# Performance work log

Measured on AMD Instinct MI355X. Metric: run time of the kernel, lower is better.

The kernel has to match this reference:

```python
import jax, jax.numpy as jnp
import numpy as np

EPS = 1e-8  # torch F.cosine_similarity default eps


def _cos_gram(x):
    # row-normalize with eps-clamped norms, then Gram matrix [N, N]
    norms = jnp.maximum(jnp.linalg.norm(x, axis=1, keepdims=True), EPS)
    xn = x / norms
    return xn @ xn.T


def setup_inputs() -> dict:
    key = jax.random.key(0)
    k1, k2 = jax.random.split(key)
    N, D = 8192, 128
    return {
        "feat_q": jax.random.normal(k1, (N, D), dtype=jnp.float32),
        "feat_k": jax.random.normal(k2, (N, D), dtype=jnp.float32),
    }


def reference(feat_q, feat_k):
    feat_k = jax.lax.stop_gradient(feat_k)  # feat_k.detach()
    N = feat_q.shape[0]
    qsim = _cos_gram(feat_q)  # [N, N]
    ksim = _cos_gram(feat_k)  # [N, N]
    # mean of (qsim - ksim)^2 over all off-diagonal (i != j) pairs
    diff2 = (qsim - ksim) ** 2
    off_diag = ~jnp.eye(N, dtype=bool)
    denom = jnp.asarray(N * (N - 1), dtype=diff2.dtype)
    loss = jnp.sum(jnp.where(off_diag, diff2, 0.0)) / denom
    return loss
```

## Files before the change

kernel.cpp:

```cpp
#include <hip/hip_runtime.h>
#include <hip/hip_bf16.h>

#define NROWS 8192
#define DDIM  128
#define NKCH  64
#define CHN   128
#define NPAIR 10
#define GB_BLOCKS 160
#define NPAD  38

typedef unsigned short ushort_t;
typedef unsigned int   uint_t;
typedef __attribute__((ext_vector_type(8))) short short8;
typedef __attribute__((ext_vector_type(4))) float floatx4;

#define LDS_PTR(p) ((__attribute__((address_space(3))) void*)(p))
#define GLB_PTR(p) ((const __attribute__((address_space(1))) void*)(p))

static __device__ inline ushort_t f2bf(float f) {
    union { float f; uint_t u; } a; a.f = f;
    uint_t u = a.u + 0x7fffu + ((a.u >> 16) & 1u);
    return (ushort_t)(u >> 16);
}

static __device__ inline void pair_decode(int p, int* ti, int* tj) {
    int i = 0, len = 4;
    while (p >= len) { p -= len; len--; i++; }
    *ti = i; *tj = i + p;
}

__global__ __launch_bounds__(256) void norm_t_kernel(
    const float* __restrict__ q, const float* __restrict__ k,
    ushort_t* __restrict__ Gt, double* acc, uint_t* counter)
{
    __shared__ ushort_t lds[256 * NPAD];
    if (blockIdx.x == 0 && threadIdx.x == 0) { *acc = 0.0; *counter = 0u; }

    int b   = blockIdx.x;
    int c   = b >> 2;
    int sub = b & 3;
    int w   = threadIdx.x >> 6;
    int l   = threadIdx.x & 63;
    int h   = l >> 5;
    int li  = l & 31;

    #pragma unroll
    for (int i = 0; i < 4; ++i) {
        int rl  = i * 8 + w * 2 + h;
        int row = b * 32 + rl;
        {
            float4 v = ((const float4*)(q + (size_t)row * DDIM))[li];
            float ss = v.x * v.x + v.y * v.y + v.z * v.z + v.w * v.w;
            #pragma unroll
            for (int o = 16; o > 0; o >>= 1) ss += __shfl_xor(ss, o, 64);
            float inv = rsqrtf(fmaxf(ss, 1e-16f));
            lds[(4 * li + 0) * NPAD + rl] = f2bf(v.x * inv);
            lds[(4 * li + 1) * NPAD + rl] = f2bf(v.y * inv);
            lds[(4 * li + 2) * NPAD + rl] = f2bf(v.z * inv);
            lds[(4 * li + 3) * NPAD + rl] = f2bf(v.w * inv);
        }
        {
            float4 v = ((const float4*)(k + (size_t)row * DDIM))[li];
            float ss = v.x * v.x + v.y * v.y + v.z * v.z + v.w * v.w;
            #pragma unroll
            for (int o = 16; o > 0; o >>= 1) ss += __shfl_xor(ss, o, 64);
            float inv = rsqrtf(fmaxf(ss, 1e-16f));
            lds[(128 + 4 * li + 0) * NPAD + rl] = f2bf(v.x * inv);
            lds[(128 + 4 * li + 1) * NPAD + rl] = f2bf(v.y * inv);
            lds[(128 + 4 * li + 2) * NPAD + rl] = f2bf(v.z * inv);
            lds[(128 + 4 * li + 3) * NPAD + rl] = f2bf(v.w * inv);
        }
    }
    __syncthreads();

    int a = threadIdx.x;
    union { uint_t u32[16]; uint4 v4[4]; } tb;
    #pragma unroll
    for (int t = 0; t < 16; ++t)
        tb.u32[t] = *(const uint_t*)&lds[a * NPAD + 2 * t];

    char* gdst = (char*)Gt + (size_t)(c * 256 + a) * (CHN * 2) + sub * 64;
    #pragma unroll
    for (int g = 0; g < 4; ++g)
        *(uint4*)(gdst + g * 16) = tb.v4[g];
}

__global__ __launch_bounds__(128, 2) void gram_a_kernel(
    const ushort_t* __restrict__ Gt, float* __restrict__ P)
{
    __shared__ ushort_t sA[64 * CHN];
    __shared__ ushort_t sB[64 * CHN];

    int pair = blockIdx.x >> 6;
    int c    = blockIdx.x & 63;
    int ti, tj;
    pair_decode(pair, &ti, &tj);
    int tid = threadIdx.x;

    const char* gA = (const char*)Gt + (size_t)(c * 256 + ti * 64) * (CHN * 2);
    const char* gB = (const char*)Gt + (size_t)(c * 256 + tj * 64) * (CHN * 2);

    #pragma unroll
    for (int it = 0; it < 8; ++it) {
        int ch = it * 128 + tid;
        int row = ch >> 4, phys = ch & 15;
        int logical = phys ^ (row & 7);
        __builtin_amdgcn_global_load_lds(GLB_PTR(gA + row * 256 + logical * 16),
                                         LDS_PTR((char*)sA + ch * 16), 16, 0, 0);
    }
    #pragma unroll
    for (int it = 0; it < 8; ++it) {
        int ch = it * 128 + tid;
        int row = ch >> 4, phys = ch & 15;
        int logical = phys ^ (row & 7);
        __builtin_amdgcn_global_load_lds(GLB_PTR(gB + row * 256 + logical * 16),
                                         LDS_PTR((char*)sB + ch * 16), 16, 0, 0);
    }
    __syncthreads();

    int w    = tid >> 6;
    int l    = tid & 63;
    int m    = l & 15;
    int quad = l >> 4;

    floatx4 accC[2][4];
    #pragma unroll
    for (int at = 0; at < 2; ++at)
        #pragma unroll
        for (int bt = 0; bt < 4; ++bt)
            accC[at][bt] = (floatx4){0.f, 0.f, 0.f, 0.f};

    #pragma unroll
    for (int kp = 0; kp < 4; ++kp) {
        short8 af[2], bf[4];
        #pragma unroll
        for (int at = 0; at < 2; ++at) {
            int ra   = w * 32 + at * 16 + m;
            int phys = (kp * 4 + quad) ^ (ra & 7);
            af[at] = *(const short8*)&sA[ra * CHN + phys * 8];
        }
        #pragma unroll
        for (int bt = 0; bt < 4; ++bt) {
            int rb   = bt * 16 + m;
            int phys = (kp * 4 + quad) ^ (rb & 7);
            bf[bt] = *(const short8*)&sB[rb * CHN + phys * 8];
        }
        #pragma unroll
        for (int at = 0; at < 2; ++at)
            #pragma unroll
            for (int bt = 0; bt < 4; ++bt)
                accC[at][bt] = __builtin_amdgcn_mfma_f32_16x16x32_bf16(af[at], bf[bt], accC[at][bt], 0, 0, 0);
    }

    float* pt = P + ((size_t)pair * NKCH + c) * 4096;
    #pragma unroll
    for (int at = 0; at < 2; ++at)
        #pragma unroll
        for (int bt = 0; bt < 4; ++bt)
            #pragma unroll
            for (int r = 0; r < 4; ++r) {
                int row = w * 32 + at * 16 + quad * 4 + r;
                int col = bt * 16 + m;
                pt[row * 64 + col] = accC[at][bt][r];
            }
}

__global__ __launch_bounds__(256) void gram_b_kernel(
    const float* __restrict__ P, double* acc, uint_t* counter, float* out)
{
    __shared__ float wsum[4];
    int e    = blockIdx.x * 256 + threadIdx.x;
    int pair = e >> 12;
    int idx  = e & 4095;

    float s = 0.f;
    #pragma unroll
    for (int c = 0; c < NKCH; ++c)
        s += P[((size_t)pair * NKCH + c) * 4096 + idx];

    int ti, tj;
    pair_decode(pair, &ti, &tj);
    float wgt = ((ti < 2) == (tj < 2)) ? 1.f : -1.f;
    if (ti != tj) wgt *= 2.f;
    float v = wgt * s * s;

    int w = threadIdx.x >> 6, l = threadIdx.x & 63;
    #pragma unroll
    for (int o = 32; o > 0; o >>= 1) v += __shfl_xor(v, o, 64);
    if (l == 0) wsum[w] = v;
    __syncthreads();
    if (threadIdx.x == 0) {
        double t = (double)wsum[0] + (double)wsum[1] + (double)wsum[2] + (double)wsum[3];
        atomicAdd(acc, t);
        __threadfence();
        uint_t old = atomicAdd(counter, 1u);
        if (old == GB_BLOCKS - 1) {
            double total = atomicAdd(acc, 0.0);
            out[0] = (float)(total * (1.0 / ((double)NROWS * (double)(NROWS - 1))));
        }
    }
}

extern "C" void kernel_launch(void* const* d_in, const int* in_sizes, int n_in,
                              void* d_out, int out_size, void* d_ws, size_t ws_size,
                              hipStream_t stream) {
    const float* q = (const float*)d_in[0];
    const float* k = (const float*)d_in[1];
    float* out = (float*)d_out;

    double*   acc = (double*)d_ws;
    uint_t*   cnt = (uint_t*)((char*)d_ws + 64);
    ushort_t* Gt  = (ushort_t*)((char*)d_ws + 256);
    float*    P   = (float*)((char*)d_ws + 256 + (size_t)NKCH * 256 * CHN * 2);

    norm_t_kernel<<<NROWS / 32, 256, 0, stream>>>(q, k, Gt, acc, cnt);
    gram_a_kernel<<<NPAIR * NKCH, 128, 0, stream>>>(Gt, P);
    gram_b_kernel<<<GB_BLOCKS, 256, 0, stream>>>(P, acc, cnt, out);
}
```

Before: 74.64 us.

## Fuse chunk reduction into gram kernel with atomics and double-buffered chunk loads

Replaces the partial-product buffer and the separate reduction kernel. Each gram block now handles four K-chunks, double-buffering their LDS loads, and accumulates its 64x64 tile into a small shared matrix with float atomics. The last block to finish computes the weighted sum of squares. The norm kernel is retiled to 16 rows per block and zeroes the accumulation matrix. This removes one launch and the large write and re-read of partials, at the cost of heavy atomic contention (16 blocks per element) and a serial final reduction run by a single block.

```diff
diff --git a/kernel.cpp b/kernel.cpp
--- a/kernel.cpp
+++ b/kernel.cpp
@@ -6,8 +6,10 @@
 #define NKCH  64
 #define CHN   128
 #define NPAIR 10
-#define GB_BLOCKS 160
-#define NPAD  38
+#define NGRP  16
+#define CPG   4
+#define K2_BLOCKS (NPAIR * NGRP)
+#define NPAD1 18
 
 typedef unsigned short ushort_t;
 typedef unsigned int   uint_t;
@@ -31,33 +33,34 @@
 
 __global__ __launch_bounds__(256) void norm_t_kernel(
     const float* __restrict__ q, const float* __restrict__ k,
-    ushort_t* __restrict__ Gt, double* acc, uint_t* counter)
+    ushort_t* __restrict__ Gt, float* __restrict__ M, uint_t* counter)
 {
-    __shared__ ushort_t lds[256 * NPAD];
-    if (blockIdx.x == 0 && threadIdx.x == 0) { *acc = 0.0; *counter = 0u; }
+    __shared__ ushort_t lds[256 * NPAD1];
+    if (blockIdx.x < K2_BLOCKS) M[blockIdx.x * 256 + threadIdx.x] = 0.f;
+    if (blockIdx.x == 0 && threadIdx.x == 0) *counter = 0u;
 
     int b   = blockIdx.x;
-    int c   = b >> 2;
-    int sub = b & 3;
+    int c   = b >> 3;
+    int sub = b & 7;
     int w   = threadIdx.x >> 6;
     int l   = threadIdx.x & 63;
     int h   = l >> 5;
     int li  = l & 31;
 
     #pragma unroll
-    for (int i = 0; i < 4; ++i) {
+    for (int i = 0; i < 2; ++i) {
         int rl  = i * 8 + w * 2 + h;
-        int row = b * 32 + rl;
+        int row = b * 16 + rl;
         {
             float4 v = ((const float4*)(q + (size_t)row * DDIM))[li];
             float ss = v.x * v.x + v.y * v.y + v.z * v.z + v.w * v.w;
             #pragma unroll
             for (int o = 16; o > 0; o >>= 1) ss += __shfl_xor(ss, o, 64);
             float inv = rsqrtf(fmaxf(ss, 1e-16f));
-            lds[(4 * li + 0) * NPAD + rl] = f2bf(v.x * inv);
-            lds[(4 * li + 1) * NPAD + rl] = f2bf(v.y * inv);
-            lds[(4 * li + 2) * NPAD + rl] = f2bf(v.z * inv);
-            lds[(4 * li + 3) * NPAD + rl] = f2bf(v.w * inv);
+            lds[(4 * li + 0) * NPAD1 + rl] = f2bf(v.x * inv);
+            lds[(4 * li + 1) * NPAD1 + rl] = f2bf(v.y * inv);
+            lds[(4 * li + 2) * NPAD1 + rl] = f2bf(v.z * inv);
+            lds[(4 * li + 3) * NPAD1 + rl] = f2bf(v.w * inv);
         }
         {
             float4 v = ((const float4*)(k + (size_t)row * DDIM))[li];
@@ -65,58 +68,61 @@
             #pragma unroll
             for (int o = 16; o > 0; o >>= 1) ss += __shfl_xor(ss, o, 64);
             float inv = rsqrtf(fmaxf(ss, 1e-16f));
-            lds[(128 + 4 * li + 0) * NPAD + rl] = f2bf(v.x * inv);
-            lds[(128 + 4 * li + 1) * NPAD + rl] = f2bf(v.y * inv);
-            lds[(128 + 4 * li + 2) * NPAD + rl] = f2bf(v.z * inv);
-            lds[(128 + 4 * li + 3) * NPAD + rl] = f2bf(v.w * inv);
+            lds[(128 + 4 * li + 0) * NPAD1 + rl] = f2bf(v.x * inv);
+            lds[(128 + 4 * li + 1) * NPAD1 + rl] = f2bf(v.y * inv);
+            lds[(128 + 4 * li + 2) * NPAD1 + rl] = f2bf(v.z * inv);
+            lds[(128 + 4 * li + 3) * NPAD1 + rl] = f2bf(v.w * inv);
         }
     }
     __syncthreads();
 
     int a = threadIdx.x;
-    union { uint_t u32[16]; uint4 v4[4]; } tb;
-    #pragma unroll
-    for (int t = 0; t < 16; ++t)
-        tb.u32[t] = *(const uint_t*)&lds[a * NPAD + 2 * t];
-
-    char* gdst = (char*)Gt + (size_t)(c * 256 + a) * (CHN * 2) + sub * 64;
-    #pragma unroll
-    for (int g = 0; g < 4; ++g)
-        *(uint4*)(gdst + g * 16) = tb.v4[g];
-}
-
-__global__ __launch_bounds__(128, 2) void gram_a_kernel(
-    const ushort_t* __restrict__ Gt, float* __restrict__ P)
+    union { uint_t u32[8]; uint4 v4[2]; } tb;
+    #pragma unroll
+    for (int t = 0; t < 8; ++t)
+        tb.u32[t] = *(const uint_t*)&lds[a * NPAD1 + 2 * t];
+
+    char* gdst = (char*)Gt + (size_t)(c * 256 + a) * (CHN * 2) + sub * 32;
+    *(uint4*)(gdst)      = tb.v4[0];
+    *(uint4*)(gdst + 16) = tb.v4[1];
+}
+
+__global__ __launch_bounds__(128) void gram_acc_kernel(
+    const ushort_t* __restrict__ Gt, float* __restrict__ M,
+    uint_t* __restrict__ counter, float* __restrict__ out)
 {
-    __shared__ ushort_t sA[64 * CHN];
-    __shared__ ushort_t sB[64 * CHN];
-
-    int pair = blockIdx.x >> 6;
-    int c    = blockIdx.x & 63;
+    __shared__ ushort_t sA[2][64 * CHN];
+    __shared__ ushort_t sB[2][64 * CHN];
+    __shared__ double dred[2];
+    __shared__ uint_t isLast;
+
+    int pair = blockIdx.x >> 4;
+    int g    = blockIdx.x & 15;
     int ti, tj;
     pair_decode(pair, &ti, &tj);
     int tid = threadIdx.x;
-
-    const char* gA = (const char*)Gt + (size_t)(c * 256 + ti * 64) * (CHN * 2);
-    const char* gB = (const char*)Gt + (size_t)(c * 256 + tj * 64) * (CHN * 2);
-
-    #pragma unroll
-    for (int it = 0; it < 8; ++it) {
-        int ch = it * 128 + tid;
-        int row = ch >> 4, phys = ch & 15;
-        int logical = phys ^ (row & 7);
-        __builtin_amdgcn_global_load_lds(GLB_PTR(gA + row * 256 + logical * 16),
-                                         LDS_PTR((char*)sA + ch * 16), 16, 0, 0);
-    }
-    #pragma unroll
-    for (int it = 0; it < 8; ++it) {
-        int ch = it * 128 + tid;
-        int row = ch >> 4, phys = ch & 15;
-        int logical = phys ^ (row & 7);
-        __builtin_amdgcn_global_load_lds(GLB_PTR(gB + row * 256 + logical * 16),
-                                         LDS_PTR((char*)sB + ch * 16), 16, 0, 0);
-    }
-    __syncthreads();
+    int c0  = g * CPG;
+
+    auto stage = [&](int buf, int c) {
+        const char* gA = (const char*)Gt + (size_t)(c * 256 + ti * 64) * (CHN * 2);
+        const char* gB = (const char*)Gt + (size_t)(c * 256 + tj * 64) * (CHN * 2);
+        #pragma unroll
+        for (int it = 0; it < 8; ++it) {
+            int ch = it * 128 + tid;
+            int row = ch >> 4, phys = ch & 15;
+            int logical = phys ^ (row & 7);
+            __builtin_amdgcn_global_load_lds(GLB_PTR(gA + row * 256 + logical * 16),
+                                             LDS_PTR((char*)sA[buf] + ch * 16), 16, 0, 0);
+        }
+        #pragma unroll
+        for (int it = 0; it < 8; ++it) {
+            int ch = it * 128 + tid;
+            int row = ch >> 4, phys = ch & 15;
+            int logical = phys ^ (row & 7);
+            __builtin_amdgcn_global_load_lds(GLB_PTR(gB + row * 256 + logical * 16),
+                                             LDS_PTR((char*)sB[buf] + ch * 16), 16, 0, 0);
+        }
+    };
 
     int w    = tid >> 6;
     int l    = tid & 63;
@@ -130,29 +136,39 @@
         for (int bt = 0; bt < 4; ++bt)
             accC[at][bt] = (floatx4){0.f, 0.f, 0.f, 0.f};
 
-    #pragma unroll
-    for (int kp = 0; kp < 4; ++kp) {
-        short8 af[2], bf[4];
-        #pragma unroll
-        for (int at = 0; at < 2; ++at) {
-            int ra   = w * 32 + at * 16 + m;
-            int phys = (kp * 4 + quad) ^ (ra & 7);
-            af[at] = *(const short8*)&sA[ra * CHN + phys * 8];
-        }
-        #pragma unroll
-        for (int bt = 0; bt < 4; ++bt) {
-            int rb   = bt * 16 + m;
-            int phys = (kp * 4 + quad) ^ (rb & 7);
-            bf[bt] = *(const short8*)&sB[rb * CHN + phys * 8];
-        }
-        #pragma unroll
-        for (int at = 0; at < 2; ++at)
-            #pragma unroll
-            for (int bt = 0; bt < 4; ++bt)
-                accC[at][bt] = __builtin_amdgcn_mfma_f32_16x16x32_bf16(af[at], bf[bt], accC[at][bt], 0, 0, 0);
-    }
-
-    float* pt = P + ((size_t)pair * NKCH + c) * 4096;
+    stage(0, c0);
+    __syncthreads();
+
+    #pragma unroll
+    for (int j = 0; j < CPG; ++j) {
+        if (j + 1 < CPG) stage((j + 1) & 1, c0 + j + 1);
+        const ushort_t* cA = sA[j & 1];
+        const ushort_t* cB = sB[j & 1];
+        #pragma unroll
+        for (int kp = 0; kp < 4; ++kp) {
+            short8 af[2], bf[4];
+            #pragma unroll
+            for (int at = 0; at < 2; ++at) {
+                int ra   = w * 32 + at * 16 + m;
+                int phys = (kp * 4 + quad) ^ (ra & 7);
+                af[at] = *(const short8*)&cA[ra * CHN + phys * 8];
+            }
+            #pragma unroll
+            for (int bt = 0; bt < 4; ++bt) {
+                int rb   = bt * 16 + m;
+                int phys = (kp * 4 + quad) ^ (rb & 7);
+                bf[bt] = *(const short8*)&cB[rb * CHN + phys * 8];
+            }
+            #pragma unroll
+            for (int at = 0; at < 2; ++at)
+                #pragma unroll
+                for (int bt = 0; bt < 4; ++bt)
+                    accC[at][bt] = __builtin_amdgcn_mfma_f32_16x16x32_bf16(af[at], bf[bt], accC[at][bt], 0, 0, 0);
+        }
+        __syncthreads();
+    }
+
+    float* mp = M + (size_t)pair * 4096;
     #pragma unroll
     for (int at = 0; at < 2; ++at)
         #pragma unroll
@@ -161,43 +177,38 @@
             for (int r = 0; r < 4; ++r) {
                 int row = w * 32 + at * 16 + quad * 4 + r;
                 int col = bt * 16 + m;
-                pt[row * 64 + col] = accC[at][bt][r];
-            }
-}
-
-__global__ __launch_bounds__(256) void gram_b_kernel(
-    const float* __restrict__ P, double* acc, uint_t* counter, float* out)
-{
-    __shared__ float wsum[4];
-    int e    = blockIdx.x * 256 + threadIdx.x;
-    int pair = e >> 12;
-    int idx  = e & 4095;
-
-    float s = 0.f;
-    #pragma unroll
-    for (int c = 0; c < NKCH; ++c)
-        s += P[((size_t)pair * NKCH + c) * 4096 + idx];
-
-    int ti, tj;
-    pair_decode(pair, &ti, &tj);
-    float wgt = ((ti < 2) == (tj < 2)) ? 1.f : -1.f;
-    if (ti != tj) wgt *= 2.f;
-    float v = wgt * s * s;
-
-    int w = threadIdx.x >> 6, l = threadIdx.x & 63;
-    #pragma unroll
-    for (int o = 32; o > 0; o >>= 1) v += __shfl_xor(v, o, 64);
-    if (l == 0) wsum[w] = v;
-    __syncthreads();
-    if (threadIdx.x == 0) {
-        double t = (double)wsum[0] + (double)wsum[1] + (double)wsum[2] + (double)wsum[3];
-        atomicAdd(acc, t);
+                atomicAdd(&mp[row * 64 + col], accC[at][bt][r]);
+            }
+
+    __syncthreads();
+    if (tid == 0) {
         __threadfence();
         uint_t old = atomicAdd(counter, 1u);
-        if (old == GB_BLOCKS - 1) {
-            double total = atomicAdd(acc, 0.0);
-            out[0] = (float)(total * (1.0 / ((double)NROWS * (double)(NROWS - 1))));
-        }
+        isLast = (old == K2_BLOCKS - 1) ? 1u : 0u;
+    }
+    __syncthreads();
+
+    if (isLast) {
+        __threadfence();
+        const float WGTS[NPAIR] = {1.f, 2.f, -2.f, -2.f, 1.f, -2.f, -2.f, 1.f, 2.f, 1.f};
+        double tacc = 0.0;
+        #pragma unroll
+        for (int p = 0; p < NPAIR; ++p) {
+            float wp = WGTS[p];
+            #pragma unroll 8
+            for (int ii = 0; ii < 32; ++ii) {
+                float s = __hip_atomic_load(&M[p * 4096 + ii * 128 + tid],
+                                            __ATOMIC_RELAXED, __HIP_MEMORY_SCOPE_AGENT);
+                tacc += (double)(wp * s * s);
+            }
+        }
+        #pragma unroll
+        for (int o = 32; o > 0; o >>= 1) tacc += __shfl_xor(tacc, o, 64);
+        if (l == 0) dred[w] = tacc;
+        __syncthreads();
+        if (tid == 0)
+            out[0] = (float)((dred[0] + dred[1]) *
+                             (1.0 / ((double)NROWS * (double)(NROWS - 1))));
     }
 }
 
@@ -208,12 +219,10 @@
     const float* k = (const float*)d_in[1];
     float* out = (float*)d_out;
 
-    double*   acc = (double*)d_ws;
-    uint_t*   cnt = (uint_t*)((char*)d_ws + 64);
-    ushort_t* Gt  = (ushort_t*)((char*)d_ws + 256);
-    float*    P   = (float*)((char*)d_ws + 256 + (size_t)NKCH * 256 * CHN * 2);
-
-    norm_t_kernel<<<NROWS / 32, 256, 0, stream>>>(q, k, Gt, acc, cnt);
-    gram_a_kernel<<<NPAIR * NKCH, 128, 0, stream>>>(Gt, P);
-    gram_b_kernel<<<GB_BLOCKS, 256, 0, stream>>>(P, acc, cnt, out);
-}
+    uint_t*   cnt = (uint_t*)d_ws;
+    float*    M   = (float*)((char*)d_ws + 256);
+    ushort_t* Gt  = (ushort_t*)((char*)d_ws + 256 + NPAIR * 4096 * 4);
+
+    norm_t_kernel<<<NROWS / 16, 256, 0, stream>>>(q, k, Gt, M, cnt);
+    gram_acc_kernel<<<K2_BLOCKS, 128, 0, stream>>>(Gt, M, cnt, out);
+}
```

New measurement: 84.33 us. 13.0% more time.

## Accumulate two K-chunks per gram block with double-buffered LDS staging

Applied to the files above, without the earlier changes.

Each gram_a block now processes two consecutive 128-row chunks with double-buffered LDS. The next chunk's global-to-LDS loads are issued while the current chunk's MFMAs run. This halves the partial-product buffer P and the reduction work in gram_b, and drops gram_a to 320 blocks. The normalization kernel is also split into twice as many blocks of 16 rows each, with a smaller LDS pad. The tradeoff is fewer blocks on the GPU and double the LDS per block, which may reduce occupancy.

```diff
diff --git a/kernel.cpp b/kernel.cpp
--- a/kernel.cpp
+++ b/kernel.cpp
@@ -6,8 +6,11 @@
 #define NKCH  64
 #define CHN   128
 #define NPAIR 10
+#define NGRP  32
+#define CPG   2
+#define K2_BLOCKS (NPAIR * NGRP)
 #define GB_BLOCKS 160
-#define NPAD  38
+#define NPAD1 18
 
 typedef unsigned short ushort_t;
 typedef unsigned int   uint_t;
@@ -33,31 +36,31 @@
     const float* __restrict__ q, const float* __restrict__ k,
     ushort_t* __restrict__ Gt, double* acc, uint_t* counter)
 {
-    __shared__ ushort_t lds[256 * NPAD];
+    __shared__ ushort_t lds[256 * NPAD1];
     if (blockIdx.x == 0 && threadIdx.x == 0) { *acc = 0.0; *counter = 0u; }
 
     int b   = blockIdx.x;
-    int c   = b >> 2;
-    int sub = b & 3;
+    int c   = b >> 3;
+    int sub = b & 7;
     int w   = threadIdx.x >> 6;
     int l   = threadIdx.x & 63;
     int h   = l >> 5;
     int li  = l & 31;
 
     #pragma unroll
-    for (int i = 0; i < 4; ++i) {
+    for (int i = 0; i < 2; ++i) {
         int rl  = i * 8 + w * 2 + h;
-        int row = b * 32 + rl;
+        int row = b * 16 + rl;
         {
             float4 v = ((const float4*)(q + (size_t)row * DDIM))[li];
             float ss = v.x * v.x + v.y * v.y + v.z * v.z + v.w * v.w;
             #pragma unroll
             for (int o = 16; o > 0; o >>= 1) ss += __shfl_xor(ss, o, 64);
             float inv = rsqrtf(fmaxf(ss, 1e-16f));
-            lds[(4 * li + 0) * NPAD + rl] = f2bf(v.x * inv);
-            lds[(4 * li + 1) * NPAD + rl] = f2bf(v.y * inv);
-            lds[(4 * li + 2) * NPAD + rl] = f2bf(v.z * inv);
-            lds[(4 * li + 3) * NPAD + rl] = f2bf(v.w * inv);
+            lds[(4 * li + 0) * NPAD1 + rl] = f2bf(v.x * inv);
+            lds[(4 * li + 1) * NPAD1 + rl] = f2bf(v.y * inv);
+            lds[(4 * li + 2) * NPAD1 + rl] = f2bf(v.z * inv);
+            lds[(4 * li + 3) * NPAD1 + rl] = f2bf(v.w * inv);
         }
         {
             float4 v = ((const float4*)(k + (size_t)row * DDIM))[li];
@@ -65,58 +68,58 @@
             #pragma unroll
             for (int o = 16; o > 0; o >>= 1) ss += __shfl_xor(ss, o, 64);
             float inv = rsqrtf(fmaxf(ss, 1e-16f));
-            lds[(128 + 4 * li + 0) * NPAD + rl] = f2bf(v.x * inv);
-            lds[(128 + 4 * li + 1) * NPAD + rl] = f2bf(v.y * inv);
-            lds[(128 + 4 * li + 2) * NPAD + rl] = f2bf(v.z * inv);
-            lds[(128 + 4 * li + 3) * NPAD + rl] = f2bf(v.w * inv);
+            lds[(128 + 4 * li + 0) * NPAD1 + rl] = f2bf(v.x * inv);
+            lds[(128 + 4 * li + 1) * NPAD1 + rl] = f2bf(v.y * inv);
+            lds[(128 + 4 * li + 2) * NPAD1 + rl] = f2bf(v.z * inv);
+            lds[(128 + 4 * li + 3) * NPAD1 + rl] = f2bf(v.w * inv);
         }
     }
     __syncthreads();
 
     int a = threadIdx.x;
-    union { uint_t u32[16]; uint4 v4[4]; } tb;
-    #pragma unroll
-    for (int t = 0; t < 16; ++t)
-        tb.u32[t] = *(const uint_t*)&lds[a * NPAD + 2 * t];
-
-    char* gdst = (char*)Gt + (size_t)(c * 256 + a) * (CHN * 2) + sub * 64;
-    #pragma unroll
-    for (int g = 0; g < 4; ++g)
-        *(uint4*)(gdst + g * 16) = tb.v4[g];
+    union { uint_t u32[8]; uint4 v4[2]; } tb;
+    #pragma unroll
+    for (int t = 0; t < 8; ++t)
+        tb.u32[t] = *(const uint_t*)&lds[a * NPAD1 + 2 * t];
+
+    char* gdst = (char*)Gt + (size_t)(c * 256 + a) * (CHN * 2) + sub * 32;
+    *(uint4*)(gdst)      = tb.v4[0];
+    *(uint4*)(gdst + 16) = tb.v4[1];
 }
 
 __global__ __launch_bounds__(128, 2) void gram_a_kernel(
     const ushort_t* __restrict__ Gt, float* __restrict__ P)
 {
-    __shared__ ushort_t sA[64 * CHN];
-    __shared__ ushort_t sB[64 * CHN];
-
-    int pair = blockIdx.x >> 6;
-    int c    = blockIdx.x & 63;
+    __shared__ ushort_t sA[2][64 * CHN];
+    __shared__ ushort_t sB[2][64 * CHN];
+
+    int pair = blockIdx.x >> 5;
+    int g    = blockIdx.x & 31;
     int ti, tj;
     pair_decode(pair, &ti, &tj);
     int tid = threadIdx.x;
-
-    const char* gA = (const char*)Gt + (size_t)(c * 256 + ti * 64) * (CHN * 2);
-    const char* gB = (const char*)Gt + (size_t)(c * 256 + tj * 64) * (CHN * 2);
-
-    #pragma unroll
-    for (int it = 0; it < 8; ++it) {
-        int ch = it * 128 + tid;
-        int row = ch >> 4, phys = ch & 15;
-        int logical = phys ^ (row & 7);
-        __builtin_amdgcn_global_load_lds(GLB_PTR(gA + row * 256 + logical * 16),
-                                         LDS_PTR((char*)sA + ch * 16), 16, 0, 0);
-    }
-    #pragma unroll
-    for (int it = 0; it < 8; ++it) {
-        int ch = it * 128 + tid;
-        int row = ch >> 4, phys = ch & 15;
-        int logical = phys ^ (row & 7);
-        __builtin_amdgcn_global_load_lds(GLB_PTR(gB + row * 256 + logical * 16),
-                                         LDS_PTR((char*)sB + ch * 16), 16, 0, 0);
-    }
-    __syncthreads();
+    int c0  = g * CPG;
+
+    auto stage = [&](int buf, int c) {
+        const char* gA = (const char*)Gt + (size_t)(c * 256 + ti * 64) * (CHN * 2);
+        const char* gB = (const char*)Gt + (size_t)(c * 256 + tj * 64) * (CHN * 2);
+        #pragma unroll
+        for (int it = 0; it < 8; ++it) {
+            int ch = it * 128 + tid;
+            int row = ch >> 4, phys = ch & 15;
+            int logical = phys ^ (row & 7);
+            __builtin_amdgcn_global_load_lds(GLB_PTR(gA + row * 256 + logical * 16),
+                                             LDS_PTR((char*)sA[buf] + ch * 16), 16, 0, 0);
+        }
+        #pragma unroll
+        for (int it = 0; it < 8; ++it) {
+            int ch = it * 128 + tid;
+            int row = ch >> 4, phys = ch & 15;
+            int logical = phys ^ (row & 7);
+            __builtin_amdgcn_global_load_lds(GLB_PTR(gB + row * 256 + logical * 16),
+                                             LDS_PTR((char*)sB[buf] + ch * 16), 16, 0, 0);
+        }
+    };
 
     int w    = tid >> 6;
     int l    = tid & 63;
@@ -130,29 +133,39 @@
         for (int bt = 0; bt < 4; ++bt)
             accC[at][bt] = (floatx4){0.f, 0.f, 0.f, 0.f};
 
-    #pragma unroll
-    for (int kp = 0; kp < 4; ++kp) {
-        short8 af[2], bf[4];
-        #pragma unroll
-        for (int at = 0; at < 2; ++at) {
-            int ra   = w * 32 + at * 16 + m;
-            int phys = (kp * 4 + quad) ^ (ra & 7);
-            af[at] = *(const short8*)&sA[ra * CHN + phys * 8];
-        }
-        #pragma unroll
-        for (int bt = 0; bt < 4; ++bt) {
-            int rb   = bt * 16 + m;
-            int phys = (kp * 4 + quad) ^ (rb & 7);
-            bf[bt] = *(const short8*)&sB[rb * CHN + phys * 8];
-        }
-        #pragma unroll
-        for (int at = 0; at < 2; ++at)
-            #pragma unroll
-            for (int bt = 0; bt < 4; ++bt)
-                accC[at][bt] = __builtin_amdgcn_mfma_f32_16x16x32_bf16(af[at], bf[bt], accC[at][bt], 0, 0, 0);
+    stage(0, c0);
+    __syncthreads();
+
+    #pragma unroll
+    for (int j = 0; j < CPG; ++j) {
+        if (j + 1 < CPG) stage((j + 1) & 1, c0 + j + 1);
+        const ushort_t* cA = sA[j & 1];
+        const ushort_t* cB = sB[j & 1];
+        #pragma unroll
+        for (int kp = 0; kp < 4; ++kp) {
+            short8 af[2], bf[4];
+            #pragma unroll
+            for (int at = 0; at < 2; ++at) {
+                int ra   = w * 32 + at * 16 + m;
+                int phys = (kp * 4 + quad) ^ (ra & 7);
+                af[at] = *(const short8*)&cA[ra * CHN + phys * 8];
+            }
+            #pragma unroll
+            for (int bt = 0; bt < 4; ++bt) {
+                int rb   = bt * 16 + m;
+                int phys = (kp * 4 + quad) ^ (rb & 7);
+                bf[bt] = *(const short8*)&cB[rb * CHN + phys * 8];
+            }
+            #pragma unroll
+            for (int at = 0; at < 2; ++at)
+                #pragma unroll
+                for (int bt = 0; bt < 4; ++bt)
+                    accC[at][bt] = __builtin_amdgcn_mfma_f32_16x16x32_bf16(af[at], bf[bt], accC[at][bt], 0, 0, 0);
+        }
+        __syncthreads();
     }
 
-    float* pt = P + ((size_t)pair * NKCH + c) * 4096;
+    float* pt = P + ((size_t)pair * NGRP + g) * 4096;
     #pragma unroll
     for (int at = 0; at < 2; ++at)
         #pragma unroll
@@ -175,8 +188,8 @@
 
     float s = 0.f;
     #pragma unroll
-    for (int c = 0; c < NKCH; ++c)
-        s += P[((size_t)pair * NKCH + c) * 4096 + idx];
+    for (int g = 0; g < NGRP; ++g)
+        s += P[((size_t)pair * NGRP + g) * 4096 + idx];
 
     int ti, tj;
     pair_decode(pair, &ti, &tj);
@@ -213,7 +226,7 @@
     ushort_t* Gt  = (ushort_t*)((char*)d_ws + 256);
     float*    P   = (float*)((char*)d_ws + 256 + (size_t)NKCH * 256 * CHN * 2);
 
-    norm_t_kernel<<<NROWS / 32, 256, 0, stream>>>(q, k, Gt, acc, cnt);
-    gram_a_kernel<<<NPAIR * NKCH, 128, 0, stream>>>(Gt, P);
+    norm_t_kernel<<<NROWS / 16, 256, 0, stream>>>(q, k, Gt, acc, cnt);
+    gram_a_kernel<<<K2_BLOCKS, 128, 0, stream>>>(Gt, P);
     gram_b_kernel<<<GB_BLOCKS, 256, 0, stream>>>(P, acc, cnt, out);
 }
```

Measured after the change: 72.33 us. -3.1%, faster.
